# Optimization experiments

Measured on AMD Instinct MI355X. Metric: run time of the kernel, lower is better.

## Reference

```python
import jax, jax.numpy as jnp
import numpy as np

B, N, D = 8, 128, 512

def setup_inputs() -> dict:
    key = jax.random.key(0)
    ks = jax.random.split(key, 8)
    def lin_w(k, fan_in, shape):
        bound = 1.0 / np.sqrt(fan_in)
        return jax.random.uniform(k, shape, jnp.float32, -bound, bound)
    return {
        "features": jax.random.normal(ks[0], (B, N, D), jnp.float32),
        "positions": jax.random.uniform(ks[1], (B, N, 2), jnp.float32),
        "W1": lin_w(ks[2], 2 * D + 2, (2 * D + 2, D)),
        "b1": lin_w(ks[3], 2 * D + 2, (D,)),
        "W2": lin_w(ks[4], D, (D, D // 2)),
        "b2": lin_w(ks[5], D, (D // 2,)),
        "W3": lin_w(ks[6], D // 2, (D // 2, 4)),
        "b3": lin_w(ks[7], D // 2, (4,)),
    }

def reference(features, positions, W1, b1, W2, b2, W3, b3):
    d = features.shape[-1]
    # Split first linear: concat([f1, f2, pos_diff]) @ W1 == f1@W1a + f2@W1b + pos_diff@W1c
    W1a, W1b, W1c = W1[:d], W1[d:2 * d], W1[2 * d:]
    h1 = jnp.einsum("bnd,dk->bnk", features, W1a)          # broadcast over axis 2 (j)
    h2 = jnp.einsum("bmd,dk->bmk", features, W1b)          # broadcast over axis 1 (i)
    pos_diff = positions[:, :, None, :] - positions[:, None, :, :]  # [B,N,N,2]
    h = h1[:, :, None, :] + h2[:, None, :, :] + jnp.einsum("bnmp,pk->bnmk", pos_diff, W1c) + b1
    h = jax.nn.relu(h)
    h = jax.nn.relu(jnp.einsum("bnmk,kl->bnml", h, W2) + b2)
    return jnp.einsum("bnml,lo->bnmo", h, W3) + b3          # [B,N,N,4]
```

## Files before the change

### kernel.cpp

```cpp
#include <hip/hip_runtime.h>
#include <hip/hip_bf16.h>

typedef unsigned short u16;
typedef unsigned int u32;
typedef __attribute__((ext_vector_type(8))) short bf16x8;
typedef __attribute__((ext_vector_type(4))) float floatx4;

__device__ __forceinline__ float bflo(u32 u){ union{u32 i; float f;}v; v.i=u<<16; return v.f; }
__device__ __forceinline__ float bfhi(u32 u){ union{u32 i; float f;}v; v.i=u&0xFFFF0000u; return v.f; }
__device__ __forceinline__ u16 f2bf(float f){
    union{float f;u32 i;}v; v.f=f; u32 r=v.i+0x7FFFu+((v.i>>16)&1u); return (u16)(r>>16);
}
__device__ __forceinline__ u32 pkbf(float a, float b){
    union { __hip_bfloat162 h; u32 u; } cv;
    cv.h = __float22bfloat162_rn(float2{a, b});
    return cv.u;
}

#define DD 512
#define NTOK 128

__global__ __launch_bounds__(512) void prep_k(
    const float* __restrict__ features, const float* __restrict__ W1,
    const float* __restrict__ W2, const float* __restrict__ b1,
    u16* __restrict__ Hf1b, u16* __restrict__ Hf2, u16* __restrict__ W2T)
{
    const int z = blockIdx.z;
    const int tid = threadIdx.x;

    if (z == 2) {
        __shared__ u16 tile[32][33];
        const int tx = tid & 31, ty = tid >> 5;
        const int r0 = blockIdx.x * 32, c0 = blockIdx.y * 32;
#pragma unroll
        for (int i = 0; i < 2; ++i) {
            int r = ty + i * 16;
            tile[r][tx] = f2bf(W2[(size_t)(r0 + r) * 256 + (c0 + tx)]);
        }
        __syncthreads();
#pragma unroll
        for (int i = 0; i < 2; ++i) {
            int c = ty + i * 16;
            W2T[(size_t)(c0 + c) * 512 + (r0 + tx)] = tile[tx][c];
        }
        return;
    }

    const int bM = blockIdx.x, bN = blockIdx.y;
    u16* outp = z ? Hf2 : Hf1b;
    __shared__ __align__(16) u16 At[64 * 64];
    __shared__ __align__(16) u16 Btl[64 * 64];
    const int wid = tid >> 6, lane = tid & 63, lrow = lane & 15, quad = lane >> 4;
    const int wm = wid >> 1, wn = wid & 1;

    floatx4 acc[2];
    acc[0] = (floatx4)(0.0f); acc[1] = (floatx4)(0.0f);

    const int m = tid >> 3, seg = tid & 7, sw = m & 7;
    const int kr = tid >> 3, csB = tid & 7;

    for (int kc = 0; kc < 8; ++kc) {
        const int k0 = kc * 64;
        {
            const float4* src = (const float4*)(features + (size_t)(bM * 64 + m) * DD + k0 + seg * 8);
            float4 f0 = src[0], f1 = src[1];
            *(uint4*)(At + m * 64 + ((seg ^ sw) << 3)) =
                make_uint4(pkbf(f0.x, f0.y), pkbf(f0.z, f0.w), pkbf(f1.x, f1.y), pkbf(f1.z, f1.w));
        }
        {
            const float4* src = (const float4*)(W1 + (size_t)(z * 512 + k0 + kr) * DD + bN * 64 + csB * 8);
            float4 g0 = src[0], g1 = src[1];
            float f[8] = { g0.x, g0.y, g0.z, g0.w, g1.x, g1.y, g1.z, g1.w };
            const int chunkB = (kr >> 3), offB = kr & 7;
#pragma unroll
            for (int i = 0; i < 8; ++i) {
                int c = csB * 8 + i;
                Btl[c * 64 + ((chunkB ^ i) << 3) + offB] = f2bf(f[i]);
            }
        }
        __syncthreads();
#pragma unroll
        for (int ks = 0; ks < 2; ++ks) {
            const int ch = ks * 4 + quad;
            int r = wm * 16 + lrow;
            bf16x8 afr = *(const bf16x8*)(At + r * 64 + ((ch ^ (r & 7)) << 3));
#pragma unroll
            for (int j = 0; j < 2; ++j) {
                int c = wn * 32 + j * 16 + lrow;
                bf16x8 bfr = *(const bf16x8*)(Btl + c * 64 + ((ch ^ (c & 7)) << 3));
                acc[j] = __builtin_amdgcn_mfma_f32_16x16x32_bf16(afr, bfr, acc[j], 0, 0, 0);
            }
        }
        __syncthreads();
    }
#pragma unroll
    for (int j = 0; j < 2; ++j) {
        int col = bN * 64 + wn * 32 + j * 16 + lrow;
        float bb = z ? 0.0f : b1[col];
#pragma unroll
        for (int r = 0; r < 4; ++r) {
            int row = bM * 64 + wm * 16 + quad * 4 + r;
            outp[(size_t)row * DD + col] = f2bf(acc[j][r] + bb);
        }
    }
}

__global__ __launch_bounds__(512) void fused_main(
    const u16* __restrict__ Hf1b, const u16* __restrict__ Hf2,
    const u16* __restrict__ W2T, const float* __restrict__ W1,
    const float* __restrict__ b2, const float* __restrict__ W3,
    const float* __restrict__ b3, const float* __restrict__ positions,
    float* __restrict__ out)
{
    const int b = blockIdx.x, n = blockIdx.y;
    const int tid = threadIdx.x;
    const int base_bn = b * NTOK + n;
    const int wid = tid >> 6, lane = tid & 63, lrow = lane & 15, quad = lane >> 4;

    __shared__ __align__(16) u16 c0b[DD], c1b[DD], s1b[DD];
    __shared__ __align__(16) u16 w3t[16 * 264];
    __shared__ __align__(16) char mbuf[49152];
    u16* Atile = (u16*)mbuf;
    u16* Btile = (u16*)(mbuf + 16384);
    u16* gh    = (u16*)mbuf;

    {
        int k = tid;
        c0b[k] = f2bf(W1[(size_t)1024 * DD + k]);
        c1b[k] = f2bf(W1[(size_t)1025 * DD + k]);
        s1b[k] = Hf1b[(size_t)base_bn * DD + k];
    }
    {
        int c = tid & 15, kb2 = tid >> 4;
        int k0w = kb2 * 8;
        u32 wv[4];
#pragma unroll
        for (int p = 0; p < 4; ++p) {
            int ka = k0w + p * 2;
            u16 va = (c < 4) ? f2bf(W3[ka * 4 + c])       : (u16)0;
            u16 vb = (c < 4) ? f2bf(W3[(ka + 1) * 4 + c]) : (u16)0;
            wv[p] = (u32)va | ((u32)vb << 16);
        }
        *(uint2*)(w3t + c * 264 + k0w)     = make_uint2(wv[0], wv[1]);
        *(uint2*)(w3t + c * 264 + k0w + 4) = make_uint2(wv[2], wv[3]);
    }
    const int mrow = tid >> 2, seg = tid & 3, swA = mrow & 7;
    float px, py;
    {
        float pnx = positions[(size_t)base_bn * 2 + 0];
        float pny = positions[(size_t)base_bn * 2 + 1];
        px = pnx - positions[(size_t)(b * NTOK + mrow) * 2 + 0];
        py = pny - positions[(size_t)(b * NTOK + mrow) * 2 + 1];
    }
    const int csrc = lane >> 3, wsrc = lane & 7;
    const u16* bsrc_lane = W2T + csrc * DD + ((wsrc ^ csrc) << 3);
    __syncthreads();

    const int wm = wid >> 2, wn = wid & 3;
    floatx4 acc[4][4];
#pragma unroll
    for (int i = 0; i < 4; ++i)
#pragma unroll
        for (int j = 0; j < 4; ++j) acc[i][j] = (floatx4)(0.0f);

    const u16* hf2p = Hf2 + (size_t)(b * NTOK + mrow) * DD;

    for (int kc = 0; kc < 8; ++kc) {
        const int k0 = kc * 64;
#pragma unroll
        for (int q = 0; q < 4; ++q) {
            const int slot = wid * 4 + q;
            __builtin_amdgcn_global_load_lds(
                (const __attribute__((address_space(1))) u32*)(bsrc_lane + slot * 8 * DD + k0),
                (__attribute__((address_space(3))) u32*)(Btile + slot * 512), 16, 0, 0);
        }

        const int kb = k0 + seg * 16;
        {
            uint4 hv = *(const uint4*)(hf2p + kb);
            uint4 hw = *(const uint4*)(hf2p + kb + 8);
            uint4 sv = *(const uint4*)(s1b + kb);
            uint4 sw2 = *(const uint4*)(s1b + kb + 8);
            uint4 av = *(const uint4*)(c0b + kb);
            uint4 aw = *(const uint4*)(c0b + kb + 8);
            uint4 bv = *(const uint4*)(c1b + kb);
            uint4 bw = *(const uint4*)(c1b + kb + 8);
            auto hp = [&](u32 h, u32 s, u32 ca, u32 cb) -> u32 {
                float h0 = bflo(h) + bflo(s) + px * bflo(ca) + py * bflo(cb);
                float h1 = bfhi(h) + bfhi(s) + px * bfhi(ca) + py * bfhi(cb);
                return pkbf(fmaxf(h0, 0.0f), fmaxf(h1, 0.0f));
            };
            uint4 o0 = make_uint4(hp(hv.x, sv.x, av.x, bv.x), hp(hv.y, sv.y, av.y, bv.y),
                                  hp(hv.z, sv.z, av.z, bv.z), hp(hv.w, sv.w, av.w, bv.w));
            uint4 o1 = make_uint4(hp(hw.x, sw2.x, aw.x, bw.x), hp(hw.y, sw2.y, aw.y, bw.y),
                                  hp(hw.z, sw2.z, aw.z, bw.z), hp(hw.w, sw2.w, aw.w, bw.w));
            *(uint4*)(Atile + mrow * 64 + (((seg * 2    ) ^ swA) << 3)) = o0;
            *(uint4*)(Atile + mrow * 64 + (((seg * 2 + 1) ^ swA) << 3)) = o1;
        }
        __syncthreads();
#pragma unroll
        for (int ks = 0; ks < 2; ++ks) {
            const int ch = ks * 4 + quad;
            bf16x8 afr[4], bfr[4];
#pragma unroll
            for (int i = 0; i < 4; ++i) {
                int r = wm * 64 + i * 16 + lrow;
                afr[i] = *(const bf16x8*)(Atile + r * 64 + ((ch ^ (r & 7)) << 3));
            }
#pragma unroll
            for (int j = 0; j < 4; ++j) {
                int c = wn * 64 + j * 16 + lrow;
                bfr[j] = *(const bf16x8*)(Btile + c * 64 + ((ch ^ (c & 7)) << 3));
            }
#pragma unroll
            for (int i = 0; i < 4; ++i)
#pragma unroll
                for (int j = 0; j < 4; ++j)
                    acc[i][j] = __builtin_amdgcn_mfma_f32_16x16x32_bf16(afr[i], bfr[j], acc[i][j], 0, 0, 0);
        }
        __syncthreads();
    }

    float b2v[4];
#pragma unroll
    for (int j = 0; j < 4; ++j) b2v[j] = b2[wn * 64 + j * 16 + lrow];

    const int smrow = wid * 16;
    floatx4 acc3 = (floatx4)(0.0f);
#pragma unroll
    for (int half = 0; half < 2; ++half) {
        __syncthreads();
        if ((wn >> 1) == half) {
#pragma unroll
            for (int i = 0; i < 4; ++i)
#pragma unroll
                for (int j = 0; j < 4; ++j)
#pragma unroll
                    for (int r = 0; r < 4; ++r) {
                        int row = wm * 64 + i * 16 + quad * 4 + r;
                        int col = (wn & 1) * 64 + j * 16 + lrow;
                        gh[row * 136 + col] = f2bf(fmaxf(acc[i][j][r] + b2v[j], 0.0f));
                    }
        }
        __syncthreads();
#pragma unroll
        for (int ks = 0; ks < 4; ++ks) {
            bf16x8 gfrag = *(const bf16x8*)(gh + (smrow + lrow) * 136 + ks * 32 + quad * 8);
            bf16x8 wfrag = *(const bf16x8*)(w3t + lrow * 264 + half * 128 + ks * 32 + quad * 8);
            acc3 = __builtin_amdgcn_mfma_f32_16x16x32_bf16(gfrag, wfrag, acc3, 0, 0, 0);
        }
    }
    if (lrow < 4) {
        float bo = b3[lrow];
#pragma unroll
        for (int r = 0; r < 4; ++r) {
            int row = smrow + quad * 4 + r;
            out[(size_t)base_bn * 512 + row * 4 + lrow] = acc3[r] + bo;
        }
    }
}

extern "C" void kernel_launch(void* const* d_in, const int* in_sizes, int n_in,
                              void* d_out, int out_size, void* d_ws, size_t ws_size,
                              hipStream_t stream)
{
    const float* features  = (const float*)d_in[0];
    const float* positions = (const float*)d_in[1];
    const float* W1 = (const float*)d_in[2];
    const float* b1 = (const float*)d_in[3];
    const float* W2 = (const float*)d_in[4];
    const float* b2 = (const float*)d_in[5];
    const float* W3 = (const float*)d_in[6];
    const float* b3 = (const float*)d_in[7];
    float* out = (float*)d_out;

    char* ws = (char*)d_ws;
    u16* W2T  = (u16*)(ws);
    u16* Hf1b = (u16*)(ws + 262144);
    u16* Hf2  = (u16*)(ws + 1310720);

    prep_k<<<dim3(16, 8, 3), 512, 0, stream>>>(features, W1, W2, b1, Hf1b, Hf2, W2T);
    fused_main<<<dim3(8, 128), 512, 0, stream>>>(Hf1b, Hf2, W2T, W1, b2, W3, b3,
                                                 positions, out);
}
```

Baseline: 127.9 us.

## Split prep into transpose and GEMM kernels, using packed bf16 conversions

The prep stage is split in two. A new transpose kernel converts W1 and W2 to transposed bf16 buffers, and a GEMM kernel loads W1T tiles straight into LDS through global_load_lds instead of doing per-element scalar conversion and scattered LDS stores. The fused main kernel's hidden-layer computation is rewritten with 2-wide float vectors so the compiler can emit packed FP32 ops, and bf16 stores are packed in pairs. The cost is an extra kernel launch and a W1T workspace buffer, while the main kernel, which likely dominates runtime, changes only slightly.

```diff
diff --git a/kernel.cpp b/kernel.cpp
--- a/kernel.cpp
+++ b/kernel.cpp
@@ -5,6 +5,7 @@
 typedef unsigned int u32;
 typedef __attribute__((ext_vector_type(8))) short bf16x8;
 typedef __attribute__((ext_vector_type(4))) float floatx4;
+typedef __attribute__((ext_vector_type(2))) float f32x2;
 
 __device__ __forceinline__ float bflo(u32 u){ union{u32 i; float f;}v; v.i=u<<16; return v.f; }
 __device__ __forceinline__ float bfhi(u32 u){ union{u32 i; float f;}v; v.i=u&0xFFFF0000u; return v.f; }
@@ -20,63 +21,55 @@
 #define DD 512
 #define NTOK 128
 
-__global__ __launch_bounds__(512) void prep_k(
-    const float* __restrict__ features, const float* __restrict__ W1,
-    const float* __restrict__ W2, const float* __restrict__ b1,
-    u16* __restrict__ Hf1b, u16* __restrict__ Hf2, u16* __restrict__ W2T)
-{
-    const int z = blockIdx.z;
+__global__ __launch_bounds__(512) void prep_t(
+    const float* __restrict__ W1, const float* __restrict__ W2,
+    u16* __restrict__ W1T, u16* __restrict__ W2T)
+{
+    const int bid = blockIdx.x;
+    const float* src; u16* dst; int sstride, dstride, kt, ct;
+    if (bid < 128) { kt = bid >> 3; ct = bid & 7;  src = W1; sstride = 512; dst = W1T; dstride = 1024; }
+    else { int t = bid - 128; kt = t >> 2; ct = t & 3; src = W2; sstride = 256; dst = W2T; dstride = 512; }
+    const int cl = threadIdx.x & 63;
+    const int kchunk = (threadIdx.x >> 6) << 3;
+    const int srow = kt * 64 + kchunk, scol = ct * 64 + cl;
+    float v[8];
+#pragma unroll
+    for (int i = 0; i < 8; ++i) v[i] = src[(size_t)(srow + i) * sstride + scol];
+    uint4 o = make_uint4(pkbf(v[0], v[1]), pkbf(v[2], v[3]),
+                         pkbf(v[4], v[5]), pkbf(v[6], v[7]));
+    *(uint4*)(dst + (size_t)scol * dstride + srow) = o;
+}
+
+__global__ __launch_bounds__(512) void prep_g(
+    const float* __restrict__ features, const u16* __restrict__ W1T,
+    const float* __restrict__ b1, u16* __restrict__ Hf1b, u16* __restrict__ Hf2)
+{
+    const int bM = blockIdx.x, bN = blockIdx.y;
     const int tid = threadIdx.x;
-
-    if (z == 2) {
-        __shared__ u16 tile[32][33];
-        const int tx = tid & 31, ty = tid >> 5;
-        const int r0 = blockIdx.x * 32, c0 = blockIdx.y * 32;
-#pragma unroll
-        for (int i = 0; i < 2; ++i) {
-            int r = ty + i * 16;
-            tile[r][tx] = f2bf(W2[(size_t)(r0 + r) * 256 + (c0 + tx)]);
-        }
-        __syncthreads();
-#pragma unroll
-        for (int i = 0; i < 2; ++i) {
-            int c = ty + i * 16;
-            W2T[(size_t)(c0 + c) * 512 + (r0 + tx)] = tile[tx][c];
-        }
-        return;
-    }
-
-    const int bM = blockIdx.x, bN = blockIdx.y;
-    u16* outp = z ? Hf2 : Hf1b;
+    const int wid = tid >> 6, lane = tid & 63, lrow = lane & 15, quad = lane >> 4;
+    const int wm = wid >> 1, wn = wid & 1;
     __shared__ __align__(16) u16 At[64 * 64];
     __shared__ __align__(16) u16 Btl[64 * 64];
-    const int wid = tid >> 6, lane = tid & 63, lrow = lane & 15, quad = lane >> 4;
-    const int wm = wid >> 1, wn = wid & 1;
 
     floatx4 acc[2];
     acc[0] = (floatx4)(0.0f); acc[1] = (floatx4)(0.0f);
 
     const int m = tid >> 3, seg = tid & 7, sw = m & 7;
-    const int kr = tid >> 3, csB = tid & 7;
+    const int zoff = (bN >> 3) * 512;
+    const u16* bsrc_lane = W1T
+        + (size_t)((bN & 7) * 64 + wid * 8 + (lane >> 3)) * 1024
+        + zoff + (((lane & 7) ^ (lane >> 3)) << 3);
 
     for (int kc = 0; kc < 8; ++kc) {
         const int k0 = kc * 64;
+        __builtin_amdgcn_global_load_lds(
+            (const __attribute__((address_space(1))) u32*)(bsrc_lane + k0),
+            (__attribute__((address_space(3))) u32*)(Btl + wid * 512), 16, 0, 0);
         {
-            const float4* src = (const float4*)(features + (size_t)(bM * 64 + m) * DD + k0 + seg * 8);
-            float4 f0 = src[0], f1 = src[1];
+            const float4* srcp = (const float4*)(features + (size_t)(bM * 64 + m) * DD + k0 + seg * 8);
+            float4 f0 = srcp[0], f1 = srcp[1];
             *(uint4*)(At + m * 64 + ((seg ^ sw) << 3)) =
                 make_uint4(pkbf(f0.x, f0.y), pkbf(f0.z, f0.w), pkbf(f1.x, f1.y), pkbf(f1.z, f1.w));
-        }
-        {
-            const float4* src = (const float4*)(W1 + (size_t)(z * 512 + k0 + kr) * DD + bN * 64 + csB * 8);
-            float4 g0 = src[0], g1 = src[1];
-            float f[8] = { g0.x, g0.y, g0.z, g0.w, g1.x, g1.y, g1.z, g1.w };
-            const int chunkB = (kr >> 3), offB = kr & 7;
-#pragma unroll
-            for (int i = 0; i < 8; ++i) {
-                int c = csB * 8 + i;
-                Btl[c * 64 + ((chunkB ^ i) << 3) + offB] = f2bf(f[i]);
-            }
         }
         __syncthreads();
 #pragma unroll
@@ -93,14 +86,17 @@
         }
         __syncthreads();
     }
+    u16* outp = (bN >> 3) ? Hf2 : Hf1b;
 #pragma unroll
     for (int j = 0; j < 2; ++j) {
-        int col = bN * 64 + wn * 32 + j * 16 + lrow;
-        float bb = z ? 0.0f : b1[col];
-#pragma unroll
-        for (int r = 0; r < 4; ++r) {
+        int col = (bN & 7) * 64 + wn * 32 + j * 16 + lrow;
+        float bb = (bN >> 3) ? 0.0f : b1[col];
+#pragma unroll
+        for (int r = 0; r < 4; r += 2) {
             int row = bM * 64 + wm * 16 + quad * 4 + r;
-            outp[(size_t)row * DD + col] = f2bf(acc[j][r] + bb);
+            u32 pk = pkbf(acc[j][r] + bb, acc[j][r + 1] + bb);
+            outp[(size_t)row * DD + col] = (u16)pk;
+            outp[(size_t)(row + 1) * DD + col] = (u16)(pk >> 16);
         }
     }
 }
@@ -152,6 +148,7 @@
         px = pnx - positions[(size_t)(b * NTOK + mrow) * 2 + 0];
         py = pny - positions[(size_t)(b * NTOK + mrow) * 2 + 1];
     }
+    const f32x2 pxv = {px, px}, pyv = {py, py};
     const int csrc = lane >> 3, wsrc = lane & 7;
     const u16* bsrc_lane = W2T + csrc * DD + ((wsrc ^ csrc) << 3);
     __syncthreads();
@@ -186,9 +183,14 @@
             uint4 bv = *(const uint4*)(c1b + kb);
             uint4 bw = *(const uint4*)(c1b + kb + 8);
             auto hp = [&](u32 h, u32 s, u32 ca, u32 cb) -> u32 {
-                float h0 = bflo(h) + bflo(s) + px * bflo(ca) + py * bflo(cb);
-                float h1 = bfhi(h) + bfhi(s) + px * bfhi(ca) + py * bfhi(cb);
-                return pkbf(fmaxf(h0, 0.0f), fmaxf(h1, 0.0f));
+                f32x2 hh = {bflo(h),  bfhi(h)};
+                f32x2 ss = {bflo(s),  bfhi(s)};
+                f32x2 aa = {bflo(ca), bfhi(ca)};
+                f32x2 bb = {bflo(cb), bfhi(cb)};
+                f32x2 r = hh + ss;
+                r += pxv * aa;
+                r += pyv * bb;
+                return pkbf(fmaxf(r.x, 0.0f), fmaxf(r.y, 0.0f));
             };
             uint4 o0 = make_uint4(hp(hv.x, sv.x, av.x, bv.x), hp(hv.y, sv.y, av.y, bv.y),
                                   hp(hv.z, sv.z, av.z, bv.z), hp(hv.w, sv.w, av.w, bv.w));
@@ -236,10 +238,14 @@
 #pragma unroll
                 for (int j = 0; j < 4; ++j)
 #pragma unroll
-                    for (int r = 0; r < 4; ++r) {
-                        int row = wm * 64 + i * 16 + quad * 4 + r;
+                    for (int r = 0; r < 4; r += 2) {
+                        int row0 = wm * 64 + i * 16 + quad * 4 + r;
                         int col = (wn & 1) * 64 + j * 16 + lrow;
-                        gh[row * 136 + col] = f2bf(fmaxf(acc[i][j][r] + b2v[j], 0.0f));
+                        float v0 = fmaxf(acc[i][j][r]     + b2v[j], 0.0f);
+                        float v1 = fmaxf(acc[i][j][r + 1] + b2v[j], 0.0f);
+                        u32 pk = pkbf(v0, v1);
+                        gh[row0 * 136 + col]       = (u16)pk;
+                        gh[(row0 + 1) * 136 + col] = (u16)(pk >> 16);
                     }
         }
         __syncthreads();
@@ -278,8 +284,10 @@
     u16* W2T  = (u16*)(ws);
     u16* Hf1b = (u16*)(ws + 262144);
     u16* Hf2  = (u16*)(ws + 1310720);
-
-    prep_k<<<dim3(16, 8, 3), 512, 0, stream>>>(features, W1, W2, b1, Hf1b, Hf2, W2T);
+    u16* W1T  = (u16*)(ws + 2359296);
+
+    prep_t<<<dim3(160), 512, 0, stream>>>(W1, W2, W1T, W2T);
+    prep_g<<<dim3(16, 16), 512, 0, stream>>>(features, W1T, b1, Hf1b, Hf2);
     fused_main<<<dim3(8, 128), 512, 0, stream>>>(Hf1b, Hf2, W2T, W1, b2, W3, b3,
                                                  positions, out);
 }
```

After: 137.9 us. 1.08x slower.
